# Optimization experiments

Measured on AMD Instinct MI355X. Metric: run time of the kernel, lower is better.

Reference implementation:

```python
import jax, jax.numpy as jnp
import numpy as np
import math

B, N, D, H, K = 8, 256, 128, 256, 128


def setup_inputs() -> dict:
    key = jax.random.key(0)
    ks = jax.random.split(key, 8)
    # forward args
    x = jax.random.uniform(ks[0], (B, N, N), dtype=jnp.float32) * 3.0  # pairwise distances
    atom_embeds = jax.random.normal(ks[1], (B, N, D), dtype=jnp.float32)
    # params of nn.Linear(2D, H) and nn.Linear(H, 2) (store as [in, out])
    lim1 = 1.0 / math.sqrt(2 * D)
    W1 = jax.random.uniform(ks[2], (2 * D, H), minval=-lim1, maxval=lim1, dtype=jnp.float32)
    b1 = jax.random.uniform(ks[3], (H,), minval=-lim1, maxval=lim1, dtype=jnp.float32)
    lim2 = 1.0 / math.sqrt(H)
    W2 = jax.random.uniform(ks[4], (H, 2), minval=-lim2, maxval=lim2, dtype=jnp.float32)
    b2 = jax.random.uniform(ks[5], (2,), minval=-lim2, maxval=lim2, dtype=jnp.float32)
    # RBF params: means ~ U(0,3), temps ~ U(0.1,10)
    means = jax.random.uniform(ks[6], (K,), minval=0.0, maxval=3.0, dtype=jnp.float32)
    temps = jax.random.uniform(ks[7], (K,), minval=0.1, maxval=10.0, dtype=jnp.float32)
    return {"x": x, "atom_embeds": atom_embeds, "W1": W1, "b1": b1,
            "W2": W2, "b2": b2, "means": means, "temps": temps}


def reference(x, atom_embeds, W1, b1, W2, b2, means, temps):
    d = atom_embeds.shape[-1]
    scale = 1.0 / math.sqrt(2 * d)
    # Split-weight trick: cat([e_i, e_j]) @ W1 == e_i @ W1[:D] + e_j @ W1[D:]
    # (same math, avoids materializing the [B,N,N,2D] concat)
    hi = jnp.einsum('bnd,dh->bnh', atom_embeds, W1[:d])   # [B,N,H]
    hj = jnp.einsum('bnd,dh->bnh', atom_embeds, W1[d:])   # [B,N,H]
    h = jax.nn.relu(hi[:, :, None, :] + hj[:, None, :, :] + b1)  # [B,N,N,H]
    edge_features = (jnp.einsum('bijh,ho->bijo', h, W2) + b2) * scale  # [B,N,N,2]
    mul = edge_features[..., 0:1]   # [B,N,N,1]
    bias = edge_features[..., 1:2]  # [B,N,N,1]
    v = mul * x[..., None] + bias   # [B,N,N,1]
    temp = jnp.abs(temps)
    # RBF gaussian basis expansion -> [B,N,N,K]
    return jnp.exp(-jnp.square(v - means) * temp)
```

## Files before the change

kernel.cpp:

```cpp
#include <hip/hip_runtime.h>
#include <hip/hip_bf16.h>


#define NB 8
#define NN 256
#define ND 128
#define NH 256
#define NK 128

typedef float f32x2 __attribute__((ext_vector_type(2)));

__global__ __launch_bounds__(256) void precompute_hij(
    const float* __restrict__ atom, const float* __restrict__ W1,
    const float* __restrict__ b1,
    float* __restrict__ hi, float* __restrict__ hjbT) {
  const int h = threadIdx.x;
  const int base = blockIdx.x * 8;
  const int b  = base >> 8;
  const int j0 = base & 255;
  __shared__ float a[8][ND];
  for (int t = threadIdx.x; t < 8 * ND; t += 256) {
    a[t >> 7][t & 127] = atom[(size_t)base * ND + t];
  }
  __syncthreads();
  float acc0[8], acc1[8];
  const float bv = b1[h];
#pragma unroll
  for (int r = 0; r < 8; ++r) { acc0[r] = 0.f; acc1[r] = bv; }
  for (int d = 0; d < ND; ++d) {
    const float w0 = W1[d * NH + h];
    const float w1 = W1[(ND + d) * NH + h];
#pragma unroll
    for (int r = 0; r < 8; ++r) {
      acc0[r] = fmaf(a[r][d], w0, acc0[r]);
      acc1[r] = fmaf(a[r][d], w1, acc1[r]);
    }
  }
#pragma unroll
  for (int r = 0; r < 8; ++r) {
    hi[(size_t)(base + r) * NH + h] = acc0[r];
    hjbT[((size_t)b * NH + h) * NN + (j0 + r)] = acc1[r];
  }
}

__global__ __launch_bounds__(256) void edge_rbf(
    const float* __restrict__ x,
    const float* __restrict__ hi, const float* __restrict__ hjbT,
    const float* __restrict__ W2, const float* __restrict__ b2,
    const float* __restrict__ means, const float* __restrict__ temps,
    float* __restrict__ out) {
  const int b    = blockIdx.x & 7;
  const int i0   = (blockIdx.x >> 3) * 2;
  const int wv   = __builtin_amdgcn_readfirstlane((int)(threadIdx.x >> 6));
  const int lane = threadIdx.x & 63;
  const int row  = i0 + (wv >> 1);
  const int j0   = (wv & 1) * 128;
  const int bi   = b * NN + row;

  const float* __restrict__ hjcol = hjbT + (size_t)b * NH * NN + j0 + 2 * lane;
  const float* __restrict__ hirow = hi + (size_t)bi * NH;

  float s0a = 0.f, s1a = 0.f, s0b = 0.f, s1b = 0.f;
#pragma unroll 8
  for (int h = 0; h < NH; ++h) {
    const f32x2 hj = *reinterpret_cast<const f32x2*>(hjcol + (size_t)h * NN);
    const float hih = hirow[h];
    const float w0  = W2[2 * h];
    const float w1  = W2[2 * h + 1];
    const float a0 = fmaxf(hih + hj.x, 0.f);
    const float a1 = fmaxf(hih + hj.y, 0.f);
    s0a = fmaf(a0, w0, s0a); s1a = fmaf(a0, w1, s1a);
    s0b = fmaf(a1, w0, s0b); s1b = fmaf(a1, w1, s1b);
  }

  const float scale = 0.0625f;
  const float b20 = b2[0], b21 = b2[1];
  const f32x2 xv = *reinterpret_cast<const f32x2*>(x + (size_t)bi * NN + j0 + 2 * lane);
  const float va = fmaf((s0a + b20) * scale, xv.x, (s1a + b21) * scale);
  const float vb = fmaf((s0b + b20) * scale, xv.y, (s1b + b21) * scale);

  const float LOG2E = 1.44269504088896340736f;
  const f32x2 mk = *reinterpret_cast<const f32x2*>(means + 2 * lane);
  f32x2 tk = *reinterpret_cast<const f32x2*>(temps + 2 * lane);
  const float t0 = -fabsf(tk.x) * LOG2E;
  const float t1 = -fabsf(tk.y) * LOG2E;

  float* __restrict__ obase = out + ((size_t)bi * NN + j0) * NK + 2 * lane;
  const int va_i = __float_as_int(va);
  const int vb_i = __float_as_int(vb);

#pragma unroll 8
  for (int c = 0; c < 64; ++c) {
    const float vj0 = __int_as_float(__builtin_amdgcn_readlane(va_i, c));
    const float vj1 = __int_as_float(__builtin_amdgcn_readlane(vb_i, c));
    const float d00 = vj0 - mk.x, d01 = vj0 - mk.y;
    const float d10 = vj1 - mk.x, d11 = vj1 - mk.y;
    f32x2 e0, e1;
    e0.x = __builtin_amdgcn_exp2f(d00 * d00 * t0);
    e0.y = __builtin_amdgcn_exp2f(d01 * d01 * t1);
    e1.x = __builtin_amdgcn_exp2f(d10 * d10 * t0);
    e1.y = __builtin_amdgcn_exp2f(d11 * d11 * t1);
    *reinterpret_cast<f32x2*>(obase + (size_t)(2 * c) * NK)     = e0;
    *reinterpret_cast<f32x2*>(obase + (size_t)(2 * c + 1) * NK) = e1;
  }
}

extern "C" void kernel_launch(void* const* d_in, const int* in_sizes, int n_in,
                              void* d_out, int out_size, void* d_ws, size_t ws_size,
                              hipStream_t stream) {
  const float* x     = (const float*)d_in[0];
  const float* atom  = (const float*)d_in[1];
  const float* W1    = (const float*)d_in[2];
  const float* b1    = (const float*)d_in[3];
  const float* W2    = (const float*)d_in[4];
  const float* b2    = (const float*)d_in[5];
  const float* means = (const float*)d_in[6];
  const float* temps = (const float*)d_in[7];
  float* out = (float*)d_out;

  float* hi   = (float*)d_ws;
  float* hjbT = hi + (size_t)NB * NN * NH;

  precompute_hij<<<NB * NN / 8, 256, 0, stream>>>(atom, W1, b1, hi, hjbT);
  edge_rbf<<<NB * NN / 2, 256, 0, stream>>>(x, hi, hjbT, W2, b2, means, temps, out);
}
```

Baseline: 89.35 us.

## Split edge kernel into v computation and a streaming float4 RBF store kernel

The fused edge kernel is split in two. One kernel computes the scalar v per atom pair into a workspace buffer. A second grid-stride kernel expands each v into the 128 RBF values with float4 stores laid out contiguously. This aims to make the dominant output write fully contiguous and independent of the MLP's register pressure and occupancy. The cost is an extra launch and a small round trip of v through global memory.

```diff
diff --git a/kernel.cpp b/kernel.cpp
--- a/kernel.cpp
+++ b/kernel.cpp
@@ -8,6 +8,7 @@
 #define NH 256
 #define NK 128
 
+typedef float f32x4 __attribute__((ext_vector_type(4)));
 typedef float f32x2 __attribute__((ext_vector_type(2)));
 
 __global__ __launch_bounds__(256) void precompute_hij(
@@ -43,27 +44,26 @@
   }
 }
 
-__global__ __launch_bounds__(256) void edge_rbf(
+__global__ __launch_bounds__(256) void compute_v(
     const float* __restrict__ x,
     const float* __restrict__ hi, const float* __restrict__ hjbT,
     const float* __restrict__ W2, const float* __restrict__ b2,
-    const float* __restrict__ means, const float* __restrict__ temps,
-    float* __restrict__ out) {
+    float* __restrict__ v) {
   const int b    = blockIdx.x & 7;
   const int i0   = (blockIdx.x >> 3) * 2;
+  const int lane = threadIdx.x & 63;
   const int wv   = __builtin_amdgcn_readfirstlane((int)(threadIdx.x >> 6));
-  const int lane = threadIdx.x & 63;
   const int row  = i0 + (wv >> 1);
   const int j0   = (wv & 1) * 128;
   const int bi   = b * NN + row;
 
-  const float* __restrict__ hjcol = hjbT + (size_t)b * NH * NN + j0 + 2 * lane;
+  const float* __restrict__ hjp = hjbT + (size_t)b * NH * NN + j0 + 2 * lane;
   const float* __restrict__ hirow = hi + (size_t)bi * NH;
 
   float s0a = 0.f, s1a = 0.f, s0b = 0.f, s1b = 0.f;
 #pragma unroll 8
   for (int h = 0; h < NH; ++h) {
-    const f32x2 hj = *reinterpret_cast<const f32x2*>(hjcol + (size_t)h * NN);
+    const f32x2 hj = *reinterpret_cast<const f32x2*>(hjp + (size_t)h * NN);
     const float hih = hirow[h];
     const float w0  = W2[2 * h];
     const float w1  = W2[2 * h + 1];
@@ -76,32 +76,43 @@
   const float scale = 0.0625f;
   const float b20 = b2[0], b21 = b2[1];
   const f32x2 xv = *reinterpret_cast<const f32x2*>(x + (size_t)bi * NN + j0 + 2 * lane);
-  const float va = fmaf((s0a + b20) * scale, xv.x, (s1a + b21) * scale);
-  const float vb = fmaf((s0b + b20) * scale, xv.y, (s1b + b21) * scale);
+  f32x2 vv;
+  vv.x = fmaf((s0a + b20) * scale, xv.x, (s1a + b21) * scale);
+  vv.y = fmaf((s0b + b20) * scale, xv.y, (s1b + b21) * scale);
+  *reinterpret_cast<f32x2*>(v + (size_t)bi * NN + j0 + 2 * lane) = vv;
+}
+
+__global__ __launch_bounds__(256) void rbf_store(
+    const float* __restrict__ v,
+    const float* __restrict__ means, const float* __restrict__ temps,
+    float* __restrict__ out) {
+  const int idx = blockIdx.x * 256 + threadIdx.x;
+  const int k0  = (idx & 31) * 4;
 
   const float LOG2E = 1.44269504088896340736f;
-  const f32x2 mk = *reinterpret_cast<const f32x2*>(means + 2 * lane);
-  f32x2 tk = *reinterpret_cast<const f32x2*>(temps + 2 * lane);
-  const float t0 = -fabsf(tk.x) * LOG2E;
-  const float t1 = -fabsf(tk.y) * LOG2E;
+  const float4 mv = *reinterpret_cast<const float4*>(means + k0);
+  float4 tv = *reinterpret_cast<const float4*>(temps + k0);
+  const float t0 = -fabsf(tv.x) * LOG2E;
+  const float t1 = -fabsf(tv.y) * LOG2E;
+  const float t2 = -fabsf(tv.z) * LOG2E;
+  const float t3 = -fabsf(tv.w) * LOG2E;
 
-  float* __restrict__ obase = out + ((size_t)bi * NN + j0) * NK + 2 * lane;
-  const int va_i = __float_as_int(va);
-  const int vb_i = __float_as_int(vb);
+  const float* __restrict__ vp = v + (idx >> 5);
+  float* __restrict__ op = out + (size_t)idx * 4;
 
-#pragma unroll 8
-  for (int c = 0; c < 64; ++c) {
-    const float vj0 = __int_as_float(__builtin_amdgcn_readlane(va_i, c));
-    const float vj1 = __int_as_float(__builtin_amdgcn_readlane(vb_i, c));
-    const float d00 = vj0 - mk.x, d01 = vj0 - mk.y;
-    const float d10 = vj1 - mk.x, d11 = vj1 - mk.y;
-    f32x2 e0, e1;
-    e0.x = __builtin_amdgcn_exp2f(d00 * d00 * t0);
-    e0.y = __builtin_amdgcn_exp2f(d01 * d01 * t1);
-    e1.x = __builtin_amdgcn_exp2f(d10 * d10 * t0);
-    e1.y = __builtin_amdgcn_exp2f(d11 * d11 * t1);
-    *reinterpret_cast<f32x2*>(obase + (size_t)(2 * c) * NK)     = e0;
-    *reinterpret_cast<f32x2*>(obase + (size_t)(2 * c + 1) * NK) = e1;
+#pragma unroll 4
+  for (int s = 0; s < 32; ++s) {
+    const float vj = vp[s * 16384];
+    const float d0 = vj - mv.x;
+    const float d1 = vj - mv.y;
+    const float d2 = vj - mv.z;
+    const float d3 = vj - mv.w;
+    f32x4 e;
+    e.x = __builtin_amdgcn_exp2f(d0 * d0 * t0);
+    e.y = __builtin_amdgcn_exp2f(d1 * d1 * t1);
+    e.z = __builtin_amdgcn_exp2f(d2 * d2 * t2);
+    e.w = __builtin_amdgcn_exp2f(d3 * d3 * t3);
+    *reinterpret_cast<f32x4*>(op + (size_t)s * 2097152) = e;
   }
 }
 
@@ -120,7 +131,9 @@
 
   float* hi   = (float*)d_ws;
   float* hjbT = hi + (size_t)NB * NN * NH;
+  float* v    = hjbT + (size_t)NB * NH * NN;
 
   precompute_hij<<<NB * NN / 8, 256, 0, stream>>>(atom, W1, b1, hi, hjbT);
-  edge_rbf<<<NB * NN / 2, 256, 0, stream>>>(x, hi, hjbT, W2, b2, means, temps, out);
+  compute_v<<<NB * NN / 2, 256, 0, stream>>>(x, hi, hjbT, W2, b2, v);
+  rbf_store<<<2048, 256, 0, stream>>>(v, means, temps, out);
 }
```

Measured after the change: 99.44 us. 1.11x slower.
